# Performance work log

Measured on AMD Instinct MI355X. Metric: run time of the kernel, lower is better.

Reference implementation:

```python
import jax, jax.numpy as jnp
import numpy as np

B = 4          # batch_size (config.batch_size)
N = 17000      # num_prots (nodes per graph)
F_IN = 256     # num_features
C = 128        # out_channels
E = 2176000    # num edges (avg degree 32)
NODES = B * N


def _gcn_layer(x, W, b, src, dst, n):
    """PyG GCNConv: add self-loops, sym-normalized aggregation, then bias.
    out[i] = sum_{j->i} d_j^{-1/2} d_i^{-1/2} (x_j W) + d_i^{-1} (x_i W) + b
    with d = degree(dst) + 1 (self loop)."""
    h = x @ W  # [n, C]
    deg = jax.ops.segment_sum(jnp.ones(src.shape[0], x.dtype), dst, num_segments=n) + 1.0
    dinv = jax.lax.rsqrt(deg)  # [n]
    coef = dinv[src] * dinv[dst]                      # [E]
    agg = jax.ops.segment_sum(h[src] * coef[:, None], dst, num_segments=n)
    agg = agg + h * (dinv * dinv)[:, None]            # self-loop term
    return agg + b


def setup_inputs() -> dict:
    key = jax.random.key(0)
    ks = jax.random.split(key, 16)

    def glorot(k, shape):
        fan_in, fan_out = shape[0], shape[1]
        s = jnp.sqrt(6.0 / (fan_in + fan_out))
        return jax.random.uniform(k, shape, jnp.float32, -s, s)

    inp = {
        "x": jax.random.normal(ks[0], (NODES, F_IN), jnp.float32),
        "edge_index": jax.random.randint(ks[1], (2, E), 0, NODES, jnp.int32),
        "protein_mask": jax.random.randint(ks[2], (B, N), 0, 2, jnp.int32),
        "W1": glorot(ks[3], (F_IN, C)), "b1": jnp.zeros((C,), jnp.float32),
        "W2": glorot(ks[4], (C, C)),    "b2": jnp.zeros((C,), jnp.float32),
        "W3": glorot(ks[5], (C, C)),    "b3": jnp.zeros((C,), jnp.float32),
        "lw1": glorot(ks[6], (C, 256)), "lb1": jnp.zeros((256,), jnp.float32),
        "lw2": glorot(ks[7], (256, 64)), "lb2": jnp.zeros((64,), jnp.float32),
        "lw3": glorot(ks[8], (64, 16)),  "lb3": jnp.zeros((16,), jnp.float32),
        "lw4": glorot(ks[9], (16, 1)),   "lb4": jnp.zeros((1,), jnp.float32),
    }
    return inp


def reference(x, edge_index, protein_mask, W1, b1, W2, b2, W3, b3,
              lw1, lb1, lw2, lb2, lw3, lb3, lw4, lb4):
    src, dst = edge_index[0], edge_index[1]
    h1 = jax.nn.relu(_gcn_layer(x, W1, b1, src, dst, NODES))   # [NODES, C]
    h2 = jax.nn.relu(_gcn_layer(h1, W2, b2, src, dst, NODES))
    h3 = jax.nn.relu(_gcn_layer(h2, W3, b3, src, dst, NODES))
    s = (h1 + h2 + h3).reshape(B, N, C)                        # residual sum
    mask = protein_mask.astype(jnp.float32)                    # [B, N]
    pooled = jnp.einsum('bn,bnc->bc', mask, s)                 # masked bmm pool [B, C]
    z = jax.nn.relu(pooled @ lw1 + lb1)
    z = jax.nn.relu(z @ lw2 + lb2)
    z = jax.nn.relu(z @ lw3 + lb3)
    return z @ lw4 + lb4                                       # [B, 1]
```

## Files before the change

### kernel.cpp

```cpp
#include <hip/hip_runtime.h>
#include <hip/hip_bf16.h>
#include <cstdint>

#define F_IN 256
#define C 128
#define NBUK_MAX 320
#define CHUNK 4096
#define CAP 12288

typedef short bf8_t __attribute__((ext_vector_type(8)));
typedef float f4_t  __attribute__((ext_vector_type(4)));

static inline size_t align256(size_t x) { return (x + 255) & ~(size_t)255; }


__global__ __launch_bounds__(256) void partition_kernel(const int* __restrict__ src,
                                                        const int* __restrict__ dst,
                                                        int* __restrict__ cntb,
                                                        int2* __restrict__ ebuf, int E) {
    __shared__ int hist[NBUK_MAX];
    __shared__ int base[NBUK_MAX];
    __shared__ int gbase[NBUK_MAX];
    __shared__ int2 stage[CHUNK];
    const int tid = threadIdx.x;
    const int e0 = blockIdx.x * CHUNK;
    const int cnt = min(CHUNK, E - e0);

    for (int i = tid; i < NBUK_MAX; i += 256) hist[i] = 0;
    __syncthreads();

    int2 ev[CHUNK / 256];
    int mo[CHUNK / 256];
#pragma unroll
    for (int k = 0; k < CHUNK / 256; ++k) {
        int e = e0 + k * 256 + tid;
        if (e < E) {
            int2 v;
            v.x = src[e];
            v.y = dst[e];
            ev[k] = v;
            mo[k] = atomicAdd(&hist[v.y >> 8], 1);
        }
    }
    __syncthreads();
    if (tid < 64) {
        int acc[5];
        int s = 0;
#pragma unroll
        for (int j = 0; j < 5; ++j) {
            int idx = tid * 5 + j;
            acc[j] = s;
            s += hist[idx];
        }
        int tot = s;
#pragma unroll
        for (int d = 1; d < 64; d <<= 1) {
            int o = __shfl_up(tot, d);
            if (tid >= d) tot += o;
        }
        int excl = tot - s;
#pragma unroll
        for (int j = 0; j < 5; ++j) base[tid * 5 + j] = excl + acc[j];
    }
    __syncthreads();
    for (int i = tid; i < NBUK_MAX; i += 256) {
        int h = hist[i];
        gbase[i] = h ? atomicAdd(&cntb[i], h) : 0;
    }
    __syncthreads();
#pragma unroll
    for (int k = 0; k < CHUNK / 256; ++k) {
        int e = e0 + k * 256 + tid;
        if (e < E) stage[base[ev[k].y >> 8] + mo[k]] = ev[k];
    }
    __syncthreads();
    for (int i = tid; i < cnt; i += 256) {
        int2 e = stage[i];
        int b = e.y >> 8;
        ebuf[(size_t)b * CAP + gbase[b] + (i - base[b])] = e;
    }
}

__global__ __launch_bounds__(256) void bscan_kernel(const int* __restrict__ cntb,
                                                    int nbuk,
                                                    int* __restrict__ ebase) {
    __shared__ int sums[NBUK_MAX];
    __shared__ int base[NBUK_MAX + 1];
    const int tid = threadIdx.x;
    for (int bk = tid; bk < NBUK_MAX; bk += 256)
        sums[bk] = (bk < nbuk) ? cntb[bk] : 0;
    __syncthreads();
    if (tid < 64) {
        int acc[5];
        int s = 0;
#pragma unroll
        for (int j = 0; j < 5; ++j) {
            acc[j] = s;
            s += sums[tid * 5 + j];
        }
        int tot = s;
#pragma unroll
        for (int d = 1; d < 64; d <<= 1) {
            int o = __shfl_up(tot, d);
            if (tid >= d) tot += o;
        }
        int excl = tot - s;
#pragma unroll
        for (int j = 0; j < 5; ++j) base[tid * 5 + j] = excl + acc[j];
        if (tid == 63) base[320] = tot;
    }
    __syncthreads();
    for (int bk = tid; bk <= nbuk; bk += 256)
        ebase[bk] = base[bk];
}

__global__ __launch_bounds__(256) void csr_build_kernel(const int2* __restrict__ ebuf,
                                                        const int* __restrict__ ebase,
                                                        int* __restrict__ offs,
                                                        float* __restrict__ dinv,
                                                        int* __restrict__ csr, int nodes) {
    __shared__ int deg[256];
    __shared__ int p[256];
    __shared__ int pre[257];
    __shared__ int cur[256];
    const int b = blockIdx.x;
    const int n0 = b << 8;
    const int ncnt = min(256, nodes - n0);
    const int tid = threadIdx.x;
    const int eb = ebase[b];
    const int cntE = ebase[b + 1] - eb;
    const int2* slab = ebuf + (size_t)b * CAP;

    deg[tid] = 0;
    __syncthreads();
    for (int k = tid; k < cntE; k += 256)
        atomicAdd(&deg[slab[k].y & 255], 1);
    __syncthreads();
    p[tid] = deg[tid];
    __syncthreads();
    for (int d = 1; d < 256; d <<= 1) {
        int v = (tid >= d) ? p[tid - d] : 0;
        __syncthreads();
        p[tid] += v;
        __syncthreads();
    }
    pre[tid + 1] = p[tid];
    if (tid == 0) pre[0] = 0;
    __syncthreads();

    for (int i = tid; i <= ncnt; i += 256)
        offs[n0 + i] = eb + pre[i] + n0 + i;
    if (tid < ncnt) {
        dinv[n0 + tid] = rsqrtf((float)(deg[tid] + 1));
        csr[eb + pre[tid] + n0 + tid] = n0 + tid;
    }
    cur[tid] = 0;
    __syncthreads();
    for (int k = tid; k < cntE; k += 256) {
        int2 e = slab[k];
        int loc = e.y & 255;
        int q = atomicAdd(&cur[loc], 1);
        csr[eb + pre[loc] + n0 + loc + 1 + q] = e.x;
    }
}

static __device__ inline unsigned pack_bf16(float a, float b) {
    __hip_bfloat162 h = __float22bfloat162_rn(make_float2(a, b));
    return *(unsigned*)&h;
}

static __device__ inline void swz_one(const float* __restrict__ W,
                                      __hip_bfloat16* __restrict__ Wsw, int i) {
    int l = i & 63;
    int u = (i >> 6) & 7;
    int t = i >> 9;
    int krow = t * 32 + (l >> 4) * 8;
    int col = u * 16 + (l & 15);
    unsigned packed[4];
#pragma unroll
    for (int j = 0; j < 4; ++j) {
        float a = W[(size_t)(krow + 2 * j) * C + col];
        float b = W[(size_t)(krow + 2 * j + 1) * C + col];
        packed[j] = pack_bf16(a, b);
    }
    uint4 o = make_uint4(packed[0], packed[1], packed[2], packed[3]);
    *(uint4*)(Wsw + (size_t)i * 8) = o;
}

__global__ __launch_bounds__(256) void wswz_all_kernel(const float* __restrict__ W1,
                                                       const float* __restrict__ W2,
                                                       const float* __restrict__ W3,
                                                       __hip_bfloat16* __restrict__ Wsw1,
                                                       __hip_bfloat16* __restrict__ Wsw2,
                                                       __hip_bfloat16* __restrict__ Wsw3) {
    int i = blockIdx.x * blockDim.x + threadIdx.x;
    if (i < 4096)      swz_one(W1, Wsw1, i);
    else if (i < 6144) swz_one(W2, Wsw2, i - 4096);
    else if (i < 8192) swz_one(W3, Wsw3, i - 6144);
}


static __device__ inline bf8_t pack8(float4 u0, float4 u1) {
    union { unsigned u[4]; bf8_t v; } r;
    r.u[0] = pack_bf16(u0.x, u0.y);
    r.u[1] = pack_bf16(u0.z, u0.w);
    r.u[2] = pack_bf16(u1.x, u1.y);
    r.u[3] = pack_bf16(u1.z, u1.w);
    return r.v;
}

template <bool F32IN>
__global__ __launch_bounds__(256) void mfma_gemm_kernel(const void* __restrict__ Xv,
                                                        const __hip_bfloat16* __restrict__ Wsw,
                                                        const float* __restrict__ dinv,
                                                        __hip_bfloat16* __restrict__ G,
                                                        int M, int K) {
    __shared__ char lds[32768];
    const int tid = threadIdx.x;
    const int l = tid & 63;
    const int w = tid >> 6;
    const int lm = l & 15;
    const int lk = (l >> 4) * 8;
    const int row0 = blockIdx.x * 128 + w * 32;

    f4_t acc[2][8] = {};
    const int steps = K >> 5;

    const float* xf[2];
    const __hip_bfloat16* xb[2];
#pragma unroll
    for (int mt = 0; mt < 2; ++mt) {
        int r = min(row0 + mt * 16 + lm, M - 1);
        xf[mt] = (const float*)Xv + (size_t)r * K + lk;
        xb[mt] = (const __hip_bfloat16*)Xv + (size_t)r * K + lk;
    }

    float4 cf[2][2];
    bf8_t cb[2];
#pragma unroll
    for (int mt = 0; mt < 2; ++mt) {
        if (F32IN) {
            cf[mt][0] = *(const float4*)(xf[mt]);
            cf[mt][1] = *(const float4*)(xf[mt] + 4);
        } else {
            cb[mt] = *(const bf8_t*)(xb[mt]);
        }
    }

    for (int s = 0; s < steps; ++s) {
        if ((s & 3) == 0) {
            if (s) __syncthreads();
            const char* wsrc = (const char*)Wsw + (size_t)s * 8192;
            for (int o = tid * 16; o < 32768; o += 256 * 16)
                *(uint4*)(lds + o) = *(const uint4*)(wsrc + o);
            __syncthreads();
        }
        float4 nf[2][2];
        bf8_t nb[2];
        if (s + 1 < steps) {
#pragma unroll
            for (int mt = 0; mt < 2; ++mt) {
                if (F32IN) {
                    nf[mt][0] = *(const float4*)(xf[mt] + (s + 1) * 32);
                    nf[mt][1] = *(const float4*)(xf[mt] + (s + 1) * 32 + 4);
                } else {
                    nb[mt] = *(const bf8_t*)(xb[mt] + (s + 1) * 32);
                }
            }
        }
        bf8_t a[2];
#pragma unroll
        for (int mt = 0; mt < 2; ++mt)
            a[mt] = F32IN ? pack8(cf[mt][0], cf[mt][1]) : cb[mt];

        const char* bbase = lds + ((size_t)((s & 3) * 8) * 64 + l) * 16;
#pragma unroll
        for (int u = 0; u < 8; ++u) {
            bf8_t b = *(const bf8_t*)(bbase + (size_t)u * 64 * 16);
#pragma unroll
            for (int mt = 0; mt < 2; ++mt)
                acc[mt][u] = __builtin_amdgcn_mfma_f32_16x16x32_bf16(a[mt], b, acc[mt][u], 0, 0, 0);
        }
#pragma unroll
        for (int mt = 0; mt < 2; ++mt) {
            if (F32IN) {
                cf[mt][0] = nf[mt][0];
                cf[mt][1] = nf[mt][1];
            } else {
                cb[mt] = nb[mt];
            }
        }
    }

#pragma unroll
    for (int mt = 0; mt < 2; ++mt) {
        int rbase = row0 + mt * 16 + (l >> 4) * 4;
#pragma unroll
        for (int r = 0; r < 4; ++r) {
            int row = rbase + r;
            if (row < M) {
                float dv = dinv[row];
#pragma unroll
                for (int u = 0; u < 8; ++u) {
                    float v = acc[mt][u][r] * dv;
                    G[(size_t)row * C + u * 16 + lm] = __float2bfloat16(v);
                }
            }
        }
    }
}

__global__ __launch_bounds__(256) void agg_kernel(const __hip_bfloat16* __restrict__ G,
                                                  const int* __restrict__ csr,
                                                  const int* __restrict__ offs,
                                                  const float* __restrict__ dinv,
                                                  const float* __restrict__ bias,
                                                  __hip_bfloat16* __restrict__ A, int nodes) {
    const int node = blockIdx.x * 4 + (threadIdx.x >> 6);
    if (node >= nodes) return;
    const int l = threadIdx.x & 63;
    const int g = l >> 4;
    const unsigned qoff = (l & 15) * 16;
    const int beg = offs[node], end = offs[node + 1];
    const char* Gb = (const char*)G;
    float acc[8] = {};

    for (int base = beg; base < end; base += 64) {
        const int cnt = min(64, end - base);
        int myidx = (l < cnt) ? csr[base + l] : 0;
        int j = 0;
        for (; j + 8 <= cnt; j += 8) {
            int i0 = __shfl(myidx, j + g);
            int i1 = __shfl(myidx, j + 4 + g);
            uint4 v0 = *(const uint4*)(Gb + (((unsigned)i0 << 8) | qoff));
            uint4 v1 = *(const uint4*)(Gb + (((unsigned)i1 << 8) | qoff));
            const __hip_bfloat162* h0 = (const __hip_bfloat162*)&v0;
            const __hip_bfloat162* h1 = (const __hip_bfloat162*)&v1;
#pragma unroll
            for (int t = 0; t < 4; ++t) {
                float2 f0 = __bfloat1622float2(h0[t]);
                float2 f1 = __bfloat1622float2(h1[t]);
                acc[2 * t]     += f0.x + f1.x;
                acc[2 * t + 1] += f0.y + f1.y;
            }
        }
        for (; j < cnt; j += 4) {
            int i0 = __shfl(myidx, j + g);
            float sc = (j + g < cnt) ? 1.f : 0.f;
            uint4 v0 = *(const uint4*)(Gb + (((unsigned)i0 << 8) | qoff));
            const __hip_bfloat162* h0 = (const __hip_bfloat162*)&v0;
#pragma unroll
            for (int t = 0; t < 4; ++t) {
                float2 f0 = __bfloat1622float2(h0[t]);
                acc[2 * t]     = fmaf(f0.x, sc, acc[2 * t]);
                acc[2 * t + 1] = fmaf(f0.y, sc, acc[2 * t + 1]);
            }
        }
    }

#pragma unroll
    for (int t = 0; t < 8; ++t) {
        acc[t] += __shfl_xor(acc[t], 16);
        acc[t] += __shfl_xor(acc[t], 32);
    }

    const float d = dinv[node];
    if (g == 0) {
        float bb[8];
        *(float4*)bb       = *(const float4*)(bias + qoff / 2);
        *(float4*)(bb + 4) = *(const float4*)(bias + qoff / 2 + 4);
        unsigned pk[4];
#pragma unroll
        for (int t = 0; t < 4; ++t) {
            float x0 = fmaxf(fmaf(acc[2 * t],     d, bb[2 * t]),     0.f);
            float x1 = fmaxf(fmaf(acc[2 * t + 1], d, bb[2 * t + 1]), 0.f);
            pk[t] = pack_bf16(x0, x1);
        }
        *(uint4*)((char*)A + (size_t)node * 256 + qoff) = make_uint4(pk[0], pk[1], pk[2], pk[3]);
    }
}

__global__ __launch_bounds__(64) void pool3_kernel(const __hip_bfloat16* __restrict__ S1,
                                                   const __hip_bfloat16* __restrict__ S2,
                                                   const __hip_bfloat16* __restrict__ S3,
                                                   const int* __restrict__ mask,
                                                   float* __restrict__ pooled, int N) {
    const int b = blockIdx.y;
    const int n0 = blockIdx.x * 128;
    const int c0 = threadIdx.x * 2;
    const int lim = min(n0 + 128, N);
    float ax = 0.f, ay = 0.f;
    for (int n = n0; n < lim; ++n) {
        if (mask[b * N + n]) {
            size_t o = ((size_t)b * N + n) * C + c0;
            float2 f1 = __bfloat1622float2(*(const __hip_bfloat162*)(S1 + o));
            float2 f2 = __bfloat1622float2(*(const __hip_bfloat162*)(S2 + o));
            float2 f3 = __bfloat1622float2(*(const __hip_bfloat162*)(S3 + o));
            ax += f1.x + f2.x + f3.x;
            ay += f1.y + f2.y + f3.y;
        }
    }
    atomicAdd(&pooled[b * C + c0], ax);
    atomicAdd(&pooled[b * C + c0 + 1], ay);
}

__global__ __launch_bounds__(256) void mlp_kernel(const float* __restrict__ pooled,
        const float* __restrict__ lw1, const float* __restrict__ lb1,
        const float* __restrict__ lw2, const float* __restrict__ lb2,
        const float* __restrict__ lw3, const float* __restrict__ lb3,
        const float* __restrict__ lw4, const float* __restrict__ lb4,
        float* __restrict__ out) {
    __shared__ float p[4 * 128];
    __shared__ float z1[4 * 256];
    __shared__ float z2[4 * 64];
    __shared__ float z3[4 * 16];
    const int tid = threadIdx.x;
    for (int i = tid; i < 4 * 128; i += 256) p[i] = pooled[i];
    __syncthreads();
    for (int o = tid; o < 4 * 256; o += 256) {
        int b = o >> 8, j = o & 255;
        float s = lb1[j];
        for (int k = 0; k < 128; ++k) s += p[b * 128 + k] * lw1[k * 256 + j];
        z1[o] = fmaxf(s, 0.f);
    }
    __syncthreads();
    for (int o = tid; o < 4 * 64; o += 256) {
        int b = o >> 6, j = o & 63;
        float s = lb2[j];
        for (int k = 0; k < 256; ++k) s += z1[b * 256 + k] * lw2[k * 64 + j];
        z2[o] = fmaxf(s, 0.f);
    }
    __syncthreads();
    if (tid < 64) {
        int b = tid >> 4, j = tid & 15;
        float s = lb3[j];
        for (int k = 0; k < 64; ++k) s += z2[b * 64 + k] * lw3[k * 16 + j];
        z3[tid] = fmaxf(s, 0.f);
    }
    __syncthreads();
    if (tid < 4) {
        float s = lb4[0];
        for (int k = 0; k < 16; ++k) s += z3[tid * 16 + k] * lw4[k];
        out[tid] = s;
    }
}


extern "C" void kernel_launch(void* const* d_in, const int* in_sizes, int n_in,
                              void* d_out, int out_size, void* d_ws, size_t ws_size,
                              hipStream_t stream) {
    const float* x    = (const float*)d_in[0];
    const int*   ei   = (const int*)d_in[1];
    const int*   pmask = (const int*)d_in[2];
    const float* W1 = (const float*)d_in[3];  const float* b1 = (const float*)d_in[4];
    const float* W2 = (const float*)d_in[5];  const float* b2 = (const float*)d_in[6];
    const float* W3 = (const float*)d_in[7];  const float* b3 = (const float*)d_in[8];
    const float* lw1 = (const float*)d_in[9];  const float* lb1 = (const float*)d_in[10];
    const float* lw2 = (const float*)d_in[11]; const float* lb2 = (const float*)d_in[12];
    const float* lw3 = (const float*)d_in[13]; const float* lb3 = (const float*)d_in[14];
    const float* lw4 = (const float*)d_in[15]; const float* lb4 = (const float*)d_in[16];
    float* out = (float*)d_out;

    const int E = in_sizes[1] / 2;
    const int NODES = in_sizes[0] / F_IN;
    const int NB = 4;
    const int NPER = NODES / NB;
    const int NBUK = (NODES + 255) >> 8;
    const int NBLK = (E + CHUNK - 1) / CHUNK;
    const int* esrc = ei;
    const int* edst = ei + E;

    char* w = (char*)d_ws;
    size_t off = 0;
    auto alloc = [&](size_t bytes) -> void* {
        void* p = w + off;
        off = align256(off + bytes);
        return p;
    };
    float* dinv = (float*)alloc((size_t)NODES * 4);
    int*   offs = (int*)  alloc((size_t)(NODES + 1) * 4);
    int*   ebase = (int*) alloc((size_t)(NBUK + 1) * 4);
    int*   cntb = (int*)  alloc((size_t)NBUK * 4);
    int2*  ebuf = (int2*) alloc((size_t)NBUK * CAP * 8);
    int*   csr  = (int*)  alloc((size_t)(E + NODES) * 4);
    __hip_bfloat16* G   = (__hip_bfloat16*)alloc((size_t)NODES * C * 2);
    __hip_bfloat16* A1  = (__hip_bfloat16*)alloc((size_t)NODES * C * 2);
    __hip_bfloat16* A2  = (__hip_bfloat16*)alloc((size_t)NODES * C * 2);
    __hip_bfloat16* A3  = (__hip_bfloat16*)alloc((size_t)NODES * C * 2);
    __hip_bfloat16* Wsw1 = (__hip_bfloat16*)alloc((size_t)F_IN * C * 2);
    __hip_bfloat16* Wsw2 = (__hip_bfloat16*)alloc((size_t)C * C * 2);
    __hip_bfloat16* Wsw3 = (__hip_bfloat16*)alloc((size_t)C * C * 2);
    float* pooled = (float*)alloc((size_t)4 * C * 4);
    (void)ws_size; (void)n_in; (void)out_size;

    hipMemsetAsync(cntb,   0, (size_t)NBUK * 4, stream);
    hipMemsetAsync(pooled, 0, (size_t)4 * C * 4, stream);

    wswz_all_kernel<<<32, 256, 0, stream>>>(W1, W2, W3, Wsw1, Wsw2, Wsw3);

    partition_kernel<<<NBLK, 256, 0, stream>>>(esrc, edst, cntb, ebuf, E);
    bscan_kernel<<<1, 256, 0, stream>>>(cntb, NBUK, ebase);
    csr_build_kernel<<<NBUK, 256, 0, stream>>>(ebuf, ebase, offs, dinv, csr, NODES);

    const int gblocks128 = (NODES + 127) / 128;
    const int ablocks = (NODES + 3) / 4;

    mfma_gemm_kernel<true><<<gblocks128, 256, 0, stream>>>(x, Wsw1, dinv, G, NODES, F_IN);
    agg_kernel<<<ablocks, 256, 0, stream>>>(G, csr, offs, dinv, b1, A1, NODES);
    mfma_gemm_kernel<false><<<gblocks128, 256, 0, stream>>>(A1, Wsw2, dinv, G, NODES, C);
    agg_kernel<<<ablocks, 256, 0, stream>>>(G, csr, offs, dinv, b2, A2, NODES);
    mfma_gemm_kernel<false><<<gblocks128, 256, 0, stream>>>(A2, Wsw3, dinv, G, NODES, C);
    agg_kernel<<<ablocks, 256, 0, stream>>>(G, csr, offs, dinv, b3, A3, NODES);

    dim3 pgrid((NPER + 127) / 128, NB);
    pool3_kernel<<<pgrid, 64, 0, stream>>>(A1, A2, A3, pmask, pooled, NPER);
    mlp_kernel<<<1, 256, 0, stream>>>(pooled, lw1, lb1, lw2, lb2, lw3, lb3, lw4, lb4, out);
}
```

Measured before the change: 492.5 us.

## Fuse neighbor aggregation with next layer's GEMM and unroll gather by sixteen

Aggregation for layers 1 and 2 now runs in a kernel that also computes the next layer's weight product. Each 128-node block aggregates its rows, writes the activations, then runs the 128x128 MFMA GEMM with the weights staged in LDS. It ping-pongs through a second buffer that reuses the edge-partition buffer. This removes two kernel launches and a separate read of the activations, and the gather inner loop is unrolled to four rows per step for more loads in flight. In exchange there are only 532 blocks, each wave walks 32 nodes one after another, and the A rows written by the block are read back right after the barrier.

```diff
diff --git a/kernel.cpp b/kernel.cpp
--- a/kernel.cpp
+++ b/kernel.cpp
@@ -310,6 +310,59 @@
     }
 }
 
+static __device__ inline void unpack_add(uint4 v, float* acc) {
+    const __hip_bfloat162* hh = (const __hip_bfloat162*)&v;
+#pragma unroll
+    for (int t = 0; t < 4; ++t) {
+        float2 f = __bfloat1622float2(hh[t]);
+        acc[2 * t]     += f.x;
+        acc[2 * t + 1] += f.y;
+    }
+}
+
+static __device__ inline void gather_rows(const char* __restrict__ Gb,
+                                          const int* __restrict__ csr,
+                                          int beg, int end, int l, int g,
+                                          unsigned qoff, float* acc) {
+    for (int base = beg; base < end; base += 64) {
+        const int cnt = min(64, end - base);
+        int myidx = (l < cnt) ? csr[base + l] : 0;
+        int j = 0;
+        for (; j + 16 <= cnt; j += 16) {
+            int i0 = __shfl(myidx, j + g);
+            int i1 = __shfl(myidx, j + 4 + g);
+            int i2 = __shfl(myidx, j + 8 + g);
+            int i3 = __shfl(myidx, j + 12 + g);
+            uint4 v0 = *(const uint4*)(Gb + (((unsigned)i0 << 8) | qoff));
+            uint4 v1 = *(const uint4*)(Gb + (((unsigned)i1 << 8) | qoff));
+            uint4 v2 = *(const uint4*)(Gb + (((unsigned)i2 << 8) | qoff));
+            uint4 v3 = *(const uint4*)(Gb + (((unsigned)i3 << 8) | qoff));
+            unpack_add(v0, acc); unpack_add(v1, acc);
+            unpack_add(v2, acc); unpack_add(v3, acc);
+        }
+        if (j + 8 <= cnt) {
+            int i0 = __shfl(myidx, j + g);
+            int i1 = __shfl(myidx, j + 4 + g);
+            uint4 v0 = *(const uint4*)(Gb + (((unsigned)i0 << 8) | qoff));
+            uint4 v1 = *(const uint4*)(Gb + (((unsigned)i1 << 8) | qoff));
+            unpack_add(v0, acc); unpack_add(v1, acc);
+            j += 8;
+        }
+        for (; j < cnt; j += 4) {
+            int i0 = __shfl(myidx, j + g);
+            float sc = (j + g < cnt) ? 1.f : 0.f;
+            uint4 v0 = *(const uint4*)(Gb + (((unsigned)i0 << 8) | qoff));
+            const __hip_bfloat162* h0 = (const __hip_bfloat162*)&v0;
+#pragma unroll
+            for (int t = 0; t < 4; ++t) {
+                float2 f0 = __bfloat1622float2(h0[t]);
+                acc[2 * t]     = fmaf(f0.x, sc, acc[2 * t]);
+                acc[2 * t + 1] = fmaf(f0.y, sc, acc[2 * t + 1]);
+            }
+        }
+    }
+}
+
 __global__ __launch_bounds__(256) void agg_kernel(const __hip_bfloat16* __restrict__ G,
                                                   const int* __restrict__ csr,
                                                   const int* __restrict__ offs,
@@ -322,41 +375,8 @@
     const int g = l >> 4;
     const unsigned qoff = (l & 15) * 16;
     const int beg = offs[node], end = offs[node + 1];
-    const char* Gb = (const char*)G;
     float acc[8] = {};
-
-    for (int base = beg; base < end; base += 64) {
-        const int cnt = min(64, end - base);
-        int myidx = (l < cnt) ? csr[base + l] : 0;
-        int j = 0;
-        for (; j + 8 <= cnt; j += 8) {
-            int i0 = __shfl(myidx, j + g);
-            int i1 = __shfl(myidx, j + 4 + g);
-            uint4 v0 = *(const uint4*)(Gb + (((unsigned)i0 << 8) | qoff));
-            uint4 v1 = *(const uint4*)(Gb + (((unsigned)i1 << 8) | qoff));
-            const __hip_bfloat162* h0 = (const __hip_bfloat162*)&v0;
-            const __hip_bfloat162* h1 = (const __hip_bfloat162*)&v1;
-#pragma unroll
-            for (int t = 0; t < 4; ++t) {
-                float2 f0 = __bfloat1622float2(h0[t]);
-                float2 f1 = __bfloat1622float2(h1[t]);
-                acc[2 * t]     += f0.x + f1.x;
-                acc[2 * t + 1] += f0.y + f1.y;
-            }
-        }
-        for (; j < cnt; j += 4) {
-            int i0 = __shfl(myidx, j + g);
-            float sc = (j + g < cnt) ? 1.f : 0.f;
-            uint4 v0 = *(const uint4*)(Gb + (((unsigned)i0 << 8) | qoff));
-            const __hip_bfloat162* h0 = (const __hip_bfloat162*)&v0;
-#pragma unroll
-            for (int t = 0; t < 4; ++t) {
-                float2 f0 = __bfloat1622float2(h0[t]);
-                acc[2 * t]     = fmaf(f0.x, sc, acc[2 * t]);
-                acc[2 * t + 1] = fmaf(f0.y, sc, acc[2 * t + 1]);
-            }
-        }
-    }
+    gather_rows((const char*)G, csr, beg, end, l, g, qoff, acc);
 
 #pragma unroll
     for (int t = 0; t < 8; ++t) {
@@ -377,6 +397,98 @@
             pk[t] = pack_bf16(x0, x1);
         }
         *(uint4*)((char*)A + (size_t)node * 256 + qoff) = make_uint4(pk[0], pk[1], pk[2], pk[3]);
+    }
+}
+
+__global__ __launch_bounds__(256) void agg_gemm_kernel(const __hip_bfloat16* __restrict__ G,
+                                                       const int* __restrict__ csr,
+                                                       const int* __restrict__ offs,
+                                                       const float* __restrict__ dinv,
+                                                       const float* __restrict__ bias,
+                                                       const __hip_bfloat16* __restrict__ Wsw,
+                                                       __hip_bfloat16* __restrict__ A,
+                                                       __hip_bfloat16* __restrict__ G2,
+                                                       int nodes) {
+    __shared__ char lds[32768];
+    const int tid = threadIdx.x;
+    const int l = tid & 63;
+    const int w = tid >> 6;
+    const int g = l >> 4;
+    const unsigned qoff = (l & 15) * 16;
+    const int nbase = blockIdx.x * 128 + w * 32;
+
+    for (int o = tid * 16; o < 32768; o += 256 * 16)
+        *(uint4*)(lds + o) = *(const uint4*)((const char*)Wsw + o);
+
+    float bb[8];
+    *(float4*)bb       = *(const float4*)(bias + qoff / 2);
+    *(float4*)(bb + 4) = *(const float4*)(bias + qoff / 2 + 4);
+    for (int i = 0; i < 32; ++i) {
+        const int node = nbase + i;
+        if (node >= nodes) break;
+        const int beg = offs[node], end = offs[node + 1];
+        float acc[8] = {};
+        gather_rows((const char*)G, csr, beg, end, l, g, qoff, acc);
+#pragma unroll
+        for (int t = 0; t < 8; ++t) {
+            acc[t] += __shfl_xor(acc[t], 16);
+            acc[t] += __shfl_xor(acc[t], 32);
+        }
+        const float d = dinv[node];
+        if (g == 0) {
+            unsigned pk[4];
+#pragma unroll
+            for (int t = 0; t < 4; ++t) {
+                float x0 = fmaxf(fmaf(acc[2 * t],     d, bb[2 * t]),     0.f);
+                float x1 = fmaxf(fmaf(acc[2 * t + 1], d, bb[2 * t + 1]), 0.f);
+                pk[t] = pack_bf16(x0, x1);
+            }
+            *(uint4*)((char*)A + (size_t)node * 256 + qoff) = make_uint4(pk[0], pk[1], pk[2], pk[3]);
+        }
+    }
+
+    __syncthreads();
+
+    const int lm = l & 15;
+    const int lk = (l >> 4) * 8;
+    const int row0 = blockIdx.x * 128 + w * 32;
+    f4_t acc2[2][8] = {};
+    const __hip_bfloat16* arow[2];
+#pragma unroll
+    for (int mt = 0; mt < 2; ++mt) {
+        int r = min(row0 + mt * 16 + lm, nodes - 1);
+        arow[mt] = A + (size_t)r * C + lk;
+    }
+#pragma unroll
+    for (int s = 0; s < 4; ++s) {
+        bf8_t a[2];
+#pragma unroll
+        for (int mt = 0; mt < 2; ++mt)
+            a[mt] = *(const bf8_t*)(arow[mt] + s * 32);
+        const char* bbase = lds + ((size_t)(s * 8) * 64 + l) * 16;
+#pragma unroll
+        for (int u = 0; u < 8; ++u) {
+            bf8_t b = *(const bf8_t*)(bbase + (size_t)u * 64 * 16);
+#pragma unroll
+            for (int mt = 0; mt < 2; ++mt)
+                acc2[mt][u] = __builtin_amdgcn_mfma_f32_16x16x32_bf16(a[mt], b, acc2[mt][u], 0, 0, 0);
+        }
+    }
+#pragma unroll
+    for (int mt = 0; mt < 2; ++mt) {
+        int rbase = row0 + mt * 16 + (l >> 4) * 4;
+#pragma unroll
+        for (int r = 0; r < 4; ++r) {
+            int row = rbase + r;
+            if (row < nodes) {
+                float dv = dinv[row];
+#pragma unroll
+                for (int u = 0; u < 8; ++u) {
+                    float v = acc2[mt][u][r] * dv;
+                    G2[(size_t)row * C + u * 16 + lm] = __float2bfloat16(v);
+                }
+            }
+        }
     }
 }
 
@@ -491,6 +603,7 @@
     __hip_bfloat16* Wsw2 = (__hip_bfloat16*)alloc((size_t)C * C * 2);
     __hip_bfloat16* Wsw3 = (__hip_bfloat16*)alloc((size_t)C * C * 2);
     float* pooled = (float*)alloc((size_t)4 * C * 4);
+    __hip_bfloat16* H = (__hip_bfloat16*)ebuf;
     (void)ws_size; (void)n_in; (void)out_size;
 
     hipMemsetAsync(cntb,   0, (size_t)NBUK * 4, stream);
@@ -506,10 +619,8 @@
     const int ablocks = (NODES + 3) / 4;
 
     mfma_gemm_kernel<true><<<gblocks128, 256, 0, stream>>>(x, Wsw1, dinv, G, NODES, F_IN);
-    agg_kernel<<<ablocks, 256, 0, stream>>>(G, csr, offs, dinv, b1, A1, NODES);
-    mfma_gemm_kernel<false><<<gblocks128, 256, 0, stream>>>(A1, Wsw2, dinv, G, NODES, C);
-    agg_kernel<<<ablocks, 256, 0, stream>>>(G, csr, offs, dinv, b2, A2, NODES);
-    mfma_gemm_kernel<false><<<gblocks128, 256, 0, stream>>>(A2, Wsw3, dinv, G, NODES, C);
+    agg_gemm_kernel<<<gblocks128, 256, 0, stream>>>(G, csr, offs, dinv, b1, Wsw2, A1, H, NODES);
+    agg_gemm_kernel<<<gblocks128, 256, 0, stream>>>(H, csr, offs, dinv, b2, Wsw3, A2, G, NODES);
     agg_kernel<<<ablocks, 256, 0, stream>>>(G, csr, offs, dinv, b3, A3, NODES);
 
     dim3 pgrid((NPER + 127) / 128, NB);
```

Measured after the change: 537.0 us. 9.0% more time.
